# Kernel optimization log

Measured on AMD Instinct MI355X. Metric: run time of the kernel, lower is better.

## Reference

```python
import jax, jax.numpy as jnp
import numpy as np

N_NODES = 50000
N_EDGES = 800000
D = 128           # node feature / hidden / out_feature
E_FEAT = 16       # raw edge_attr dim
N_LAYERS = 3
BN_EPS = 1e-5
INV_SQRT2 = 0.7071067811865476


def setup_inputs() -> dict:
    key = jax.random.key(0)
    ks = jax.random.split(key, 12)
    x = jax.random.normal(ks[0], (N_NODES, D), dtype=jnp.float32)
    edge_index = jax.random.randint(ks[1], (2, N_EDGES), 0, N_NODES, dtype=jnp.int64)
    edge_attr = jax.random.normal(ks[2], (N_EDGES, E_FEAT), dtype=jnp.float32)
    edge_weight = jax.random.uniform(ks[3], (N_EDGES,), dtype=jnp.float32)
    # shared edge encoder (same module instance passed to every conv)
    We = jax.random.normal(ks[4], (E_FEAT, D), dtype=jnp.float32) * (1.0 / np.sqrt(E_FEAT))
    be = jnp.zeros((D,), dtype=jnp.float32)
    # per-layer MLP: Linear(D->D), GELU, Linear(D->D)
    W1 = jax.random.normal(ks[5], (N_LAYERS, D, D), dtype=jnp.float32) * (1.0 / np.sqrt(D))
    b1 = jnp.zeros((N_LAYERS, D), dtype=jnp.float32)
    W2 = jax.random.normal(ks[6], (N_LAYERS, D, D), dtype=jnp.float32) * (1.0 / np.sqrt(D))
    b2 = jnp.zeros((N_LAYERS, D), dtype=jnp.float32)
    eps = jnp.zeros((N_LAYERS,), dtype=jnp.float32)  # GINE eps params, init 0
    gamma = jnp.ones((N_LAYERS, D), dtype=jnp.float32)
    beta = jnp.zeros((N_LAYERS, D), dtype=jnp.float32)
    return {"x": x, "edge_index": edge_index, "edge_attr": edge_attr,
            "edge_weight": edge_weight, "We": We, "be": be, "W1": W1, "b1": b1,
            "W2": W2, "b2": b2, "eps": eps, "gamma": gamma, "beta": beta}


def reference(x, edge_index, edge_attr, edge_weight, We, be, W1, b1, W2, b2, eps, gamma, beta):
    src = edge_index[0]
    dst = edge_index[1]
    ew = edge_weight[:, None]                      # [E,1]
    edge_emb = edge_attr @ We + be                 # shared bond encoder, [E,D]
    n = x.shape[0]
    for i in range(N_LAYERS):
        # message: gelu(x_j + edge_emb) * edge_weight, scatter-add to dst
        m = jax.nn.gelu(x[src] + edge_emb, approximate=False) * ew   # [E,D]
        agg = jax.ops.segment_sum(m, dst, num_segments=n)            # [N,D]
        h = (1.0 + eps[i]) * x + agg
        h = jax.nn.gelu(h @ W1[i] + b1[i], approximate=False) @ W2[i] + b2[i]
        # BatchNorm1d, training mode (biased batch var)
        mu = jnp.mean(h, axis=0)
        var = jnp.var(h, axis=0)
        h = (h - mu) * jax.lax.rsqrt(var + BN_EPS) * gamma[i] + beta[i]
        h = jax.nn.gelu(h, approximate=False)
        # dropout p=0.0 -> identity; residual (shapes always match here)
        x = (x + h) * INV_SQRT2
    return x
```

## Files before the change

kernel.cpp:

```cpp
#include <hip/hip_runtime.h>
#include <math.h>

#define N_NODES 50000
#define N_EDGES 800000
#define D 128
#define E_FEAT 16
#define NLAYERS 3
#define BN_EPS 1e-5f
#define INV_SQRT2 0.70710678118654752f

typedef __attribute__((ext_vector_type(8))) short short8;
typedef __attribute__((ext_vector_type(4))) float f32x4;

__device__ __forceinline__ float gelu_fast(float v) {
    const float u = v * INV_SQRT2;
    const float a = __builtin_fabsf(u);
    const float t = __builtin_amdgcn_rcpf(__builtin_fmaf(0.3275911f, a, 1.0f));
    float p = __builtin_fmaf(1.061405429f, t, -1.453152027f);
    p = __builtin_fmaf(p, t, 1.421413741f);
    p = __builtin_fmaf(p, t, -0.284496736f);
    p = __builtin_fmaf(p, t, 0.254829592f);
    p = p * t;
    const float e = __builtin_amdgcn_exp2f(-1.4426950408889634f * a * a);
    const float erf_a = __builtin_fmaf(-p, e, 1.0f);
    const float erf_u = __builtin_copysignf(erf_a, u);
    return 0.5f * v * (1.0f + erf_u);
}

__device__ __forceinline__ unsigned short f2bf(float f) {
    unsigned u = __float_as_uint(f);
    unsigned r = (u + 0x7FFFu + ((u >> 16) & 1u)) >> 16;
    return (unsigned short)r;
}

__global__ __launch_bounds__(256) void count_kernel(const int* __restrict__ dst,
                                                    int* __restrict__ counts) {
    int e = blockIdx.x * 256 + threadIdx.x;
    if (e < N_EDGES) atomicAdd(&counts[dst[e]], 1);
}

#define NSCAN_BLOCKS 196
__global__ __launch_bounds__(256) void scan1_kernel(const int* __restrict__ counts,
                                                    int* __restrict__ offsets,
                                                    int* __restrict__ bsum) {
    __shared__ int wsum[4];
    __shared__ int wexcl[4];
    const int t = threadIdx.x, lane = t & 63, wid = t >> 6;
    const int idx = blockIdx.x * 256 + t;
    int v = (idx < N_NODES) ? counts[idx] : 0;
    int incl = v;
    #pragma unroll
    for (int off = 1; off < 64; off <<= 1) {
        int u = __shfl_up(incl, off, 64);
        if (lane >= off) incl += u;
    }
    if (lane == 63) wsum[wid] = incl;
    __syncthreads();
    if (t == 0) {
        int r = 0;
        #pragma unroll
        for (int g = 0; g < 4; ++g) { wexcl[g] = r; r += wsum[g]; }
        bsum[blockIdx.x] = r;
    }
    __syncthreads();
    if (idx < N_NODES) offsets[idx] = wexcl[wid] + (incl - v);
}

__global__ __launch_bounds__(256) void scan2_kernel(const int* __restrict__ bsum,
                                                    int* __restrict__ bbase,
                                                    int* __restrict__ offsets) {
    __shared__ int wsum[4];
    __shared__ int wexcl[4];
    const int t = threadIdx.x, lane = t & 63, wid = t >> 6;
    int v = (t < NSCAN_BLOCKS) ? bsum[t] : 0;
    int incl = v;
    #pragma unroll
    for (int off = 1; off < 64; off <<= 1) {
        int u = __shfl_up(incl, off, 64);
        if (lane >= off) incl += u;
    }
    if (lane == 63) wsum[wid] = incl;
    __syncthreads();
    if (t == 0) {
        int r = 0;
        #pragma unroll
        for (int g = 0; g < 4; ++g) { wexcl[g] = r; r += wsum[g]; }
        offsets[N_NODES] = r;
    }
    __syncthreads();
    if (t < NSCAN_BLOCKS) bbase[t] = wexcl[wid] + (incl - v);
}

__global__ __launch_bounds__(256) void scan3_kernel(int* __restrict__ offsets,
                                                    const int* __restrict__ bbase,
                                                    int* __restrict__ cursor) {
    const int idx = blockIdx.x * 256 + threadIdx.x;
    if (idx < N_NODES) {
        const int o = offsets[idx] + bbase[blockIdx.x];
        offsets[idx] = o;
        cursor[idx] = o;
    }
}

__global__ __launch_bounds__(256) void scatter_kernel(const int* __restrict__ dst,
                                                      int* __restrict__ cursor,
                                                      int* __restrict__ sorted_eid) {
    int e = blockIdx.x * 256 + threadIdx.x;
    if (e < N_EDGES) {
        int p = atomicAdd(&cursor[dst[e]], 1);
        sorted_eid[p] = e;
    }
}

__global__ __launch_bounds__(256) void permute_kernel(
    const int* __restrict__ sorted_eid,
    const int* __restrict__ src,
    const float* __restrict__ ew,
    const float* __restrict__ ea,
    int* __restrict__ sorted_src,
    float* __restrict__ sorted_ew,
    float* __restrict__ sorted_ea)
{
    int p = blockIdx.x * 256 + threadIdx.x;
    if (p < N_EDGES) {
        const int e = sorted_eid[p];
        sorted_src[p] = src[e];
        sorted_ew[p]  = ew[e];
        const float4* s4 = (const float4*)(ea + (size_t)e * E_FEAT);
        float4* d4 = (float4*)(sorted_ea + (size_t)p * E_FEAT);
        d4[0] = s4[0]; d4[1] = s4[1]; d4[2] = s4[2]; d4[3] = s4[3];
    }
}

__global__ __launch_bounds__(256) void pack_kernel(const float* __restrict__ W1,
                                                   const float* __restrict__ W2,
                                                   unsigned short* __restrict__ Wp) {
    const int idx = blockIdx.x * 256 + threadIdx.x;
    if (idx >= 6 * 2048) return;
    const int m    = idx >> 11;
    const int rem  = idx & 2047;
    const int ct   = rem >> 8;
    const int rem2 = rem & 255;
    const int kt   = rem2 >> 6;
    const int lane = rem2 & 63;
    const float* Wsrc = (m < 3) ? (W1 + (size_t)m * D * D)
                                : (W2 + (size_t)(m - 3) * D * D);
    const int k0  = kt * 32 + (lane >> 4) * 8;
    const int col = ct * 16 + (lane & 15);
    unsigned short o[8];
    #pragma unroll
    for (int j = 0; j < 8; ++j) o[j] = f2bf(Wsrc[(size_t)(k0 + j) * D + col]);
    unsigned short* d = Wp + (size_t)idx * 8;
    #pragma unroll
    for (int j = 0; j < 8; ++j) d[j] = o[j];
}

__global__ __launch_bounds__(256, 4) void aggregate_kernel(
    const float* __restrict__ x,
    const int* __restrict__ sorted_src,
    const float* __restrict__ sorted_ew,
    const float* __restrict__ sorted_ea,
    const int* __restrict__ offsets,
    const float* __restrict__ We,
    const float* __restrict__ be,
    const float* __restrict__ eps_p,
    float* __restrict__ pre)
{
    const int t = threadIdx.x;
    const int lane = t & 63;
    const int node = blockIdx.x * 4 + (t >> 6);
    const int c0 = lane * 2;

    float2 wreg[E_FEAT];
    #pragma unroll
    for (int k = 0; k < E_FEAT; ++k)
        wreg[k] = *(const float2*)&We[k * D + c0];
    const float2 bev = *(const float2*)&be[c0];
    const float e1 = 1.0f + *eps_p;

    const int start = __builtin_amdgcn_readfirstlane(offsets[node]);
    const int end   = __builtin_amdgcn_readfirstlane(offsets[node + 1]);

    float a0 = 0.0f, a1 = 0.0f;
    int p = start;
    for (; p + 2 <= end; p += 2) {
        const int s0 = __builtin_amdgcn_readfirstlane(sorted_src[p]);
        const int s1 = __builtin_amdgcn_readfirstlane(sorted_src[p + 1]);
        const float2 x0 = *(const float2*)&x[(size_t)s0 * D + c0];
        const float2 x1 = *(const float2*)&x[(size_t)s1 * D + c0];
        const float w0 = sorted_ew[p];
        const float w1 = sorted_ew[p + 1];
        const float* __restrict__ ea0 = sorted_ea + (size_t)p * E_FEAT;
        const float* __restrict__ ea1 = ea0 + E_FEAT;

        float m00 = bev.x, m01 = bev.y, m10 = bev.x, m11 = bev.y;
        #pragma unroll
        for (int k = 0; k < E_FEAT; ++k) {
            const float e0k = ea0[k];
            m00 = __builtin_fmaf(e0k, wreg[k].x, m00);
            m01 = __builtin_fmaf(e0k, wreg[k].y, m01);
        }
        #pragma unroll
        for (int k = 0; k < E_FEAT; ++k) {
            const float e1k = ea1[k];
            m10 = __builtin_fmaf(e1k, wreg[k].x, m10);
            m11 = __builtin_fmaf(e1k, wreg[k].y, m11);
        }
        a0 = __builtin_fmaf(gelu_fast(x0.x + m00), w0, a0);
        a1 = __builtin_fmaf(gelu_fast(x0.y + m01), w0, a1);
        a0 = __builtin_fmaf(gelu_fast(x1.x + m10), w1, a0);
        a1 = __builtin_fmaf(gelu_fast(x1.y + m11), w1, a1);
    }
    if (p < end) {
        const int s0 = __builtin_amdgcn_readfirstlane(sorted_src[p]);
        const float2 x0 = *(const float2*)&x[(size_t)s0 * D + c0];
        const float w0 = sorted_ew[p];
        const float* __restrict__ ea0 = sorted_ea + (size_t)p * E_FEAT;
        float m00 = bev.x, m01 = bev.y;
        #pragma unroll
        for (int k = 0; k < E_FEAT; ++k) {
            const float e0k = ea0[k];
            m00 = __builtin_fmaf(e0k, wreg[k].x, m00);
            m01 = __builtin_fmaf(e0k, wreg[k].y, m01);
        }
        a0 = __builtin_fmaf(gelu_fast(x0.x + m00), w0, a0);
        a1 = __builtin_fmaf(gelu_fast(x0.y + m01), w0, a1);
    }

    const float2 xnode = *(const float2*)&x[(size_t)node * D + c0];
    float2 o;
    o.x = e1 * xnode.x + a0;
    o.y = e1 * xnode.y + a1;
    *(float2*)&pre[(size_t)node * D + c0] = o;
}

#define GM 64
#define LDB 136

__global__ __launch_bounds__(256, 4) void mlp_fused_kernel(
    const float* __restrict__ pre,
    const unsigned short* __restrict__ Wp1,
    const float* __restrict__ b1,
    const unsigned short* __restrict__ Wp2,
    const float* __restrict__ b2,
    float* __restrict__ H,
    float* __restrict__ colsum,
    float* __restrict__ colsumsq)
{
    __shared__ __align__(16) unsigned short sAb[GM * LDB];
    __shared__ float sred[2][4][D];
    const int t = threadIdx.x;
    const int row0 = blockIdx.x * GM;

    for (int i = t; i < GM * (D / 4); i += 256) {
        const int r  = i / (D / 4);
        const int cc = (i % (D / 4)) * 4;
        const int gr = row0 + r;
        float4 v;
        if (gr < N_NODES) v = *(const float4*)&pre[(size_t)gr * D + cc];
        else { v.x = v.y = v.z = v.w = 0.0f; }
        ushort4 h;
        h.x = f2bf(v.x); h.y = f2bf(v.y); h.z = f2bf(v.z); h.w = f2bf(v.w);
        *(ushort4*)&sAb[r * LDB + cc] = h;
    }
    __syncthreads();

    const int wave = t >> 6, lane = t & 63;
    const int m0   = wave * 16;
    const int mrow = lane & 15;
    const int q    = lane >> 4;
    const int colb = lane & 15;

    short8 a[4];
    #pragma unroll
    for (int kt = 0; kt < 4; ++kt)
        a[kt] = *(const short8*)&sAb[(m0 + mrow) * LDB + kt * 32 + q * 8];

    f32x4 acc[8];
    #pragma unroll
    for (int ct = 0; ct < 8; ++ct) acc[ct] = (f32x4){0.f, 0.f, 0.f, 0.f};
    #pragma unroll
    for (int ct = 0; ct < 8; ++ct) {
        #pragma unroll
        for (int kt = 0; kt < 4; ++kt) {
            const short8 b = *(const short8*)&Wp1[((size_t)(ct * 4 + kt) * 64 + lane) * 8];
            acc[ct] = __builtin_amdgcn_mfma_f32_16x16x32_bf16(a[kt], b, acc[ct], 0, 0, 0);
        }
    }

    #pragma unroll
    for (int ct = 0; ct < 8; ++ct) {
        const float bb = b1[ct * 16 + colb];
        #pragma unroll
        for (int r = 0; r < 4; ++r) {
            const float o = gelu_fast(acc[ct][r] + bb);
            sAb[(m0 + q * 4 + r) * LDB + ct * 16 + colb] = f2bf(o);
        }
    }

    #pragma unroll
    for (int kt = 0; kt < 4; ++kt)
        a[kt] = *(const short8*)&sAb[(m0 + mrow) * LDB + kt * 32 + q * 8];
    #pragma unroll
    for (int ct = 0; ct < 8; ++ct) acc[ct] = (f32x4){0.f, 0.f, 0.f, 0.f};
    #pragma unroll
    for (int ct = 0; ct < 8; ++ct) {
        #pragma unroll
        for (int kt = 0; kt < 4; ++kt) {
            const short8 b = *(const short8*)&Wp2[((size_t)(ct * 4 + kt) * 64 + lane) * 8];
            acc[ct] = __builtin_amdgcn_mfma_f32_16x16x32_bf16(a[kt], b, acc[ct], 0, 0, 0);
        }
    }

    #pragma unroll
    for (int ct = 0; ct < 8; ++ct) {
        const float bb = b2[ct * 16 + colb];
        float ssum = 0.f, qsum = 0.f;
        #pragma unroll
        for (int r = 0; r < 4; ++r) {
            const int grow = row0 + m0 + q * 4 + r;
            const float o = acc[ct][r] + bb;
            if (grow < N_NODES) {
                H[(size_t)grow * D + ct * 16 + colb] = o;
                ssum += o;
                qsum += o * o;
            }
        }
        ssum += __shfl_xor(ssum, 16, 64);
        ssum += __shfl_xor(ssum, 32, 64);
        qsum += __shfl_xor(qsum, 16, 64);
        qsum += __shfl_xor(qsum, 32, 64);
        if (q == 0) {
            sred[0][wave][ct * 16 + colb] = ssum;
            sred[1][wave][ct * 16 + colb] = qsum;
        }
    }
    __syncthreads();
    if (t < D) {
        const float ss = sred[0][0][t] + sred[0][1][t] + sred[0][2][t] + sred[0][3][t];
        const float qq = sred[1][0][t] + sred[1][1][t] + sred[1][2][t] + sred[1][3][t];
        atomicAdd(&colsum[t], ss);
        atomicAdd(&colsumsq[t], qq);
    }
}

__global__ __launch_bounds__(256) void bn_apply_kernel(
    const float* __restrict__ H,
    const float* __restrict__ colsum,
    const float* __restrict__ colsumsq,
    const float* __restrict__ gamma,
    const float* __restrict__ beta,
    const float* __restrict__ x_in,
    float* __restrict__ x_out)
{
    const int idx = blockIdx.x * 256 + threadIdx.x;
    const int c0 = (idx & 31) * 4;
    const float invN = 1.0f / (float)N_NODES;

    const float4 s  = *(const float4*)&colsum[c0];
    const float4 q  = *(const float4*)&colsumsq[c0];
    const float4 g  = *(const float4*)&gamma[c0];
    const float4 bt = *(const float4*)&beta[c0];
    const float4 h  = *(const float4*)&H[(size_t)idx * 4];
    const float4 xv = *(const float4*)&x_in[(size_t)idx * 4];

    float4 o;
    {
        float mu = s.x * invN, var = q.x * invN - mu * mu;
        float hn = (h.x - mu) * rsqrtf(var + BN_EPS) * g.x + bt.x;
        o.x = (xv.x + gelu_fast(hn)) * INV_SQRT2;
    }
    {
        float mu = s.y * invN, var = q.y * invN - mu * mu;
        float hn = (h.y - mu) * rsqrtf(var + BN_EPS) * g.y + bt.y;
        o.y = (xv.y + gelu_fast(hn)) * INV_SQRT2;
    }
    {
        float mu = s.z * invN, var = q.z * invN - mu * mu;
        float hn = (h.z - mu) * rsqrtf(var + BN_EPS) * g.z + bt.z;
        o.z = (xv.z + gelu_fast(hn)) * INV_SQRT2;
    }
    {
        float mu = s.w * invN, var = q.w * invN - mu * mu;
        float hn = (h.w - mu) * rsqrtf(var + BN_EPS) * g.w + bt.w;
        o.w = (xv.w + gelu_fast(hn)) * INV_SQRT2;
    }
    *(float4*)&x_out[(size_t)idx * 4] = o;
}

extern "C" void kernel_launch(void* const* d_in, const int* in_sizes, int n_in,
                              void* d_out, int out_size, void* d_ws, size_t ws_size,
                              hipStream_t stream) {
    const float* x_in  = (const float*)d_in[0];
    const int*   ei    = (const int*)d_in[1];
    const float* ea    = (const float*)d_in[2];
    const float* ew    = (const float*)d_in[3];
    const float* We    = (const float*)d_in[4];
    const float* be    = (const float*)d_in[5];
    const float* W1    = (const float*)d_in[6];
    const float* b1    = (const float*)d_in[7];
    const float* W2    = (const float*)d_in[8];
    const float* b2    = (const float*)d_in[9];
    const float* eps   = (const float*)d_in[10];
    const float* gamma = (const float*)d_in[11];
    const float* beta  = (const float*)d_in[12];

    const int* src = ei;
    const int* dst = ei + N_EDGES;

    float* xcur = (float*)d_out;

    int*   counts       = (int*)d_ws;
    float* colsum_all   = (float*)(counts + N_NODES);
    float* colsumsq_all = colsum_all + NLAYERS * D;
    int*   cursor       = (int*)(colsumsq_all + NLAYERS * D);
    int*   offsets      = cursor + N_NODES;
    int*   bsum         = offsets + N_NODES + 4;
    int*   bbase        = bsum + 256;
    int*   sorted_eid   = bbase + 256;
    int*   sorted_src   = sorted_eid + N_EDGES;
    float* sorted_ew    = (float*)(sorted_src + N_EDGES);
    float* sorted_ea    = sorted_ew + N_EDGES;
    unsigned short* Wpack = (unsigned short*)(sorted_ea + (size_t)N_EDGES * E_FEAT);
    float* preH         = (float*)(Wpack + 6 * 2048 * 8);

    hipMemsetAsync(counts, 0, sizeof(int) * (N_NODES + 2 * NLAYERS * D), stream);
    count_kernel<<<(N_EDGES + 255) / 256, 256, 0, stream>>>(dst, counts);
    scan1_kernel<<<NSCAN_BLOCKS, 256, 0, stream>>>(counts, offsets, bsum);
    scan2_kernel<<<1, 256, 0, stream>>>(bsum, bbase, offsets);
    scan3_kernel<<<NSCAN_BLOCKS, 256, 0, stream>>>(offsets, bbase, cursor);
    scatter_kernel<<<(N_EDGES + 255) / 256, 256, 0, stream>>>(dst, cursor, sorted_eid);
    permute_kernel<<<(N_EDGES + 255) / 256, 256, 0, stream>>>(
        sorted_eid, src, ew, ea, sorted_src, sorted_ew, sorted_ea);
    pack_kernel<<<48, 256, 0, stream>>>(W1, W2, Wpack);

    const int mlp_blocks = (N_NODES + GM - 1) / GM;
    const int bn_blocks  = (N_NODES * D / 4) / 256;
    const int agg_blocks = N_NODES / 4;

    for (int i = 0; i < NLAYERS; ++i) {
        const float* xl = (i == 0) ? x_in : xcur;
        aggregate_kernel<<<agg_blocks, 256, 0, stream>>>(
            xl, sorted_src, sorted_ew, sorted_ea, offsets, We, be, eps + i, preH);
        mlp_fused_kernel<<<mlp_blocks, 256, 0, stream>>>(
            preH, Wpack + (size_t)i * 16384, b1 + (size_t)i * D,
            Wpack + (size_t)(3 + i) * 16384, b2 + (size_t)i * D,
            preH, colsum_all + i * D, colsumsq_all + i * D);
        bn_apply_kernel<<<bn_blocks, 256, 0, stream>>>(
            preH, colsum_all + i * D, colsumsq_all + i * D,
            gamma + (size_t)i * D, beta + (size_t)i * D, xl, xcur);
    }
}
```

Before: 690.0 us.

## Precompute bf16 edge embeddings once, use tanh GELU, store intermediates in bf16

Edge embeddings (edge_attr @ We + be) are now computed once, in a permute kernel, and stored sorted as packed bf16, so the three aggregate passes no longer redo the 16-wide dot product per edge. The aggregate kernel uses a tanh-based GELU approximation instead of the erf polynomial, and gets higher occupancy bounds. The pre-MLP and post-MLP activations are stored as bf16 instead of fp32, halving intermediate traffic. In exchange, each aggregate pass reads a 256-byte embedding per edge, the tanh GELU changes numerics relative to exact erf, and bf16 storage adds rounding error.

```diff
diff --git a/kernel.cpp b/kernel.cpp
--- a/kernel.cpp
+++ b/kernel.cpp
@@ -27,11 +27,22 @@
     return 0.5f * v * (1.0f + erf_u);
 }
 
+__device__ __forceinline__ float gelu_tanh(float x) {
+    const float x2 = x * x;
+    const float z = x * __builtin_fmaf(0.0356774081f, x2, 0.7978845608f);
+    const float E = __builtin_amdgcn_exp2f(z * 2.885390082f);
+    const float r = __builtin_amdgcn_rcpf(E + 1.0f);
+    const float th = __builtin_fmaf(-2.0f, r, 1.0f);
+    return 0.5f * x * (1.0f + th);
+}
+
 __device__ __forceinline__ unsigned short f2bf(float f) {
     unsigned u = __float_as_uint(f);
     unsigned r = (u + 0x7FFFu + ((u >> 16) & 1u)) >> 16;
     return (unsigned short)r;
 }
+__device__ __forceinline__ float bf2f_lo(unsigned u) { return __uint_as_float(u << 16); }
+__device__ __forceinline__ float bf2f_hi(unsigned u) { return __uint_as_float(u & 0xFFFF0000u); }
 
 __global__ __launch_bounds__(256) void count_kernel(const int* __restrict__ dst,
                                                     int* __restrict__ counts) {
@@ -112,23 +123,45 @@
     }
 }
 
-__global__ __launch_bounds__(256) void permute_kernel(
+#define PE_BLOCKS 2048
+#define PE_WAVES (PE_BLOCKS * 4)
+__global__ __launch_bounds__(256, 4) void permute_emb_kernel(
     const int* __restrict__ sorted_eid,
     const int* __restrict__ src,
     const float* __restrict__ ew,
     const float* __restrict__ ea,
+    const float* __restrict__ We,
+    const float* __restrict__ be,
     int* __restrict__ sorted_src,
     float* __restrict__ sorted_ew,
-    float* __restrict__ sorted_ea)
+    unsigned int* __restrict__ sorted_emb)
 {
-    int p = blockIdx.x * 256 + threadIdx.x;
-    if (p < N_EDGES) {
-        const int e = sorted_eid[p];
-        sorted_src[p] = src[e];
-        sorted_ew[p]  = ew[e];
-        const float4* s4 = (const float4*)(ea + (size_t)e * E_FEAT);
-        float4* d4 = (float4*)(sorted_ea + (size_t)p * E_FEAT);
-        d4[0] = s4[0]; d4[1] = s4[1]; d4[2] = s4[2]; d4[3] = s4[3];
+    const int t = threadIdx.x;
+    const int lane = t & 63;
+    const int gw = blockIdx.x * 4 + (t >> 6);
+    const int c0 = lane * 2;
+
+    float2 wreg[E_FEAT];
+    #pragma unroll
+    for (int k = 0; k < E_FEAT; ++k)
+        wreg[k] = *(const float2*)&We[k * D + c0];
+    const float2 bev = *(const float2*)&be[c0];
+
+    for (int p = gw; p < N_EDGES; p += PE_WAVES) {
+        const int eid = __builtin_amdgcn_readfirstlane(sorted_eid[p]);
+        const int s   = __builtin_amdgcn_readfirstlane(src[eid]);
+        const float w = ew[eid];
+        const float* __restrict__ ear = ea + (size_t)eid * E_FEAT;
+        float m0 = bev.x, m1 = bev.y;
+        #pragma unroll
+        for (int k = 0; k < E_FEAT; ++k) {
+            const float eak = ear[k];
+            m0 = __builtin_fmaf(eak, wreg[k].x, m0);
+            m1 = __builtin_fmaf(eak, wreg[k].y, m1);
+        }
+        const unsigned int packed = (unsigned int)f2bf(m0) | ((unsigned int)f2bf(m1) << 16);
+        sorted_emb[(size_t)p * 64 + lane] = packed;
+        if (lane == 0) { sorted_src[p] = s; sorted_ew[p] = w; }
     }
 }
 
@@ -155,27 +188,19 @@
     for (int j = 0; j < 8; ++j) d[j] = o[j];
 }
 
-__global__ __launch_bounds__(256, 4) void aggregate_kernel(
+__global__ __launch_bounds__(256, 8) void aggregate_kernel(
     const float* __restrict__ x,
     const int* __restrict__ sorted_src,
     const float* __restrict__ sorted_ew,
-    const float* __restrict__ sorted_ea,
+    const unsigned int* __restrict__ sorted_emb,
     const int* __restrict__ offsets,
-    const float* __restrict__ We,
-    const float* __restrict__ be,
     const float* __restrict__ eps_p,
-    float* __restrict__ pre)
+    unsigned int* __restrict__ preb)
 {
     const int t = threadIdx.x;
     const int lane = t & 63;
     const int node = blockIdx.x * 4 + (t >> 6);
     const int c0 = lane * 2;
-
-    float2 wreg[E_FEAT];
-    #pragma unroll
-    for (int k = 0; k < E_FEAT; ++k)
-        wreg[k] = *(const float2*)&We[k * D + c0];
-    const float2 bev = *(const float2*)&be[c0];
     const float e1 = 1.0f + *eps_p;
 
     const int start = __builtin_amdgcn_readfirstlane(offsets[node]);
@@ -188,62 +213,40 @@
         const int s1 = __builtin_amdgcn_readfirstlane(sorted_src[p + 1]);
         const float2 x0 = *(const float2*)&x[(size_t)s0 * D + c0];
         const float2 x1 = *(const float2*)&x[(size_t)s1 * D + c0];
+        const unsigned int e0 = sorted_emb[(size_t)p * 64 + lane];
+        const unsigned int e1u = sorted_emb[(size_t)(p + 1) * 64 + lane];
         const float w0 = sorted_ew[p];
         const float w1 = sorted_ew[p + 1];
-        const float* __restrict__ ea0 = sorted_ea + (size_t)p * E_FEAT;
-        const float* __restrict__ ea1 = ea0 + E_FEAT;
-
-        float m00 = bev.x, m01 = bev.y, m10 = bev.x, m11 = bev.y;
-        #pragma unroll
-        for (int k = 0; k < E_FEAT; ++k) {
-            const float e0k = ea0[k];
-            m00 = __builtin_fmaf(e0k, wreg[k].x, m00);
-            m01 = __builtin_fmaf(e0k, wreg[k].y, m01);
-        }
-        #pragma unroll
-        for (int k = 0; k < E_FEAT; ++k) {
-            const float e1k = ea1[k];
-            m10 = __builtin_fmaf(e1k, wreg[k].x, m10);
-            m11 = __builtin_fmaf(e1k, wreg[k].y, m11);
-        }
-        a0 = __builtin_fmaf(gelu_fast(x0.x + m00), w0, a0);
-        a1 = __builtin_fmaf(gelu_fast(x0.y + m01), w0, a1);
-        a0 = __builtin_fmaf(gelu_fast(x1.x + m10), w1, a0);
-        a1 = __builtin_fmaf(gelu_fast(x1.y + m11), w1, a1);
+        a0 = __builtin_fmaf(gelu_tanh(x0.x + bf2f_lo(e0)),  w0, a0);
+        a1 = __builtin_fmaf(gelu_tanh(x0.y + bf2f_hi(e0)),  w0, a1);
+        a0 = __builtin_fmaf(gelu_tanh(x1.x + bf2f_lo(e1u)), w1, a0);
+        a1 = __builtin_fmaf(gelu_tanh(x1.y + bf2f_hi(e1u)), w1, a1);
     }
     if (p < end) {
         const int s0 = __builtin_amdgcn_readfirstlane(sorted_src[p]);
         const float2 x0 = *(const float2*)&x[(size_t)s0 * D + c0];
+        const unsigned int e0 = sorted_emb[(size_t)p * 64 + lane];
         const float w0 = sorted_ew[p];
-        const float* __restrict__ ea0 = sorted_ea + (size_t)p * E_FEAT;
-        float m00 = bev.x, m01 = bev.y;
-        #pragma unroll
-        for (int k = 0; k < E_FEAT; ++k) {
-            const float e0k = ea0[k];
-            m00 = __builtin_fmaf(e0k, wreg[k].x, m00);
-            m01 = __builtin_fmaf(e0k, wreg[k].y, m01);
-        }
-        a0 = __builtin_fmaf(gelu_fast(x0.x + m00), w0, a0);
-        a1 = __builtin_fmaf(gelu_fast(x0.y + m01), w0, a1);
+        a0 = __builtin_fmaf(gelu_tanh(x0.x + bf2f_lo(e0)), w0, a0);
+        a1 = __builtin_fmaf(gelu_tanh(x0.y + bf2f_hi(e0)), w0, a1);
     }
 
     const float2 xnode = *(const float2*)&x[(size_t)node * D + c0];
-    float2 o;
-    o.x = e1 * xnode.x + a0;
-    o.y = e1 * xnode.y + a1;
-    *(float2*)&pre[(size_t)node * D + c0] = o;
+    const float o0 = __builtin_fmaf(e1, xnode.x, a0);
+    const float o1 = __builtin_fmaf(e1, xnode.y, a1);
+    preb[(size_t)node * 64 + lane] = (unsigned int)f2bf(o0) | ((unsigned int)f2bf(o1) << 16);
 }
 
 #define GM 64
 #define LDB 136
 
 __global__ __launch_bounds__(256, 4) void mlp_fused_kernel(
-    const float* __restrict__ pre,
+    const unsigned short* __restrict__ preb,
     const unsigned short* __restrict__ Wp1,
     const float* __restrict__ b1,
     const unsigned short* __restrict__ Wp2,
     const float* __restrict__ b2,
-    float* __restrict__ H,
+    unsigned short* __restrict__ Hb,
     float* __restrict__ colsum,
     float* __restrict__ colsumsq)
 {
@@ -252,16 +255,14 @@
     const int t = threadIdx.x;
     const int row0 = blockIdx.x * GM;
 
-    for (int i = t; i < GM * (D / 4); i += 256) {
-        const int r  = i / (D / 4);
-        const int cc = (i % (D / 4)) * 4;
+    for (int i = t; i < GM * (D / 8); i += 256) {
+        const int r  = i / (D / 8);
+        const int cc = (i % (D / 8)) * 8;
         const int gr = row0 + r;
-        float4 v;
-        if (gr < N_NODES) v = *(const float4*)&pre[(size_t)gr * D + cc];
-        else { v.x = v.y = v.z = v.w = 0.0f; }
-        ushort4 h;
-        h.x = f2bf(v.x); h.y = f2bf(v.y); h.z = f2bf(v.z); h.w = f2bf(v.w);
-        *(ushort4*)&sAb[r * LDB + cc] = h;
+        uint4 v;
+        if (gr < N_NODES) v = *(const uint4*)&preb[(size_t)gr * D + cc];
+        else { v.x = v.y = v.z = v.w = 0u; }
+        *(uint4*)&sAb[r * LDB + cc] = v;
     }
     __syncthreads();
 
@@ -321,7 +322,7 @@
             const int grow = row0 + m0 + q * 4 + r;
             const float o = acc[ct][r] + bb;
             if (grow < N_NODES) {
-                H[(size_t)grow * D + ct * 16 + colb] = o;
+                Hb[(size_t)grow * D + ct * 16 + colb] = f2bf(o);
                 ssum += o;
                 qsum += o * o;
             }
@@ -345,7 +346,7 @@
 }
 
 __global__ __launch_bounds__(256) void bn_apply_kernel(
-    const float* __restrict__ H,
+    const unsigned short* __restrict__ Hb,
     const float* __restrict__ colsum,
     const float* __restrict__ colsumsq,
     const float* __restrict__ gamma,
@@ -361,28 +362,32 @@
     const float4 q  = *(const float4*)&colsumsq[c0];
     const float4 g  = *(const float4*)&gamma[c0];
     const float4 bt = *(const float4*)&beta[c0];
-    const float4 h  = *(const float4*)&H[(size_t)idx * 4];
+    const ushort4 hb = *(const ushort4*)&Hb[(size_t)idx * 4];
     const float4 xv = *(const float4*)&x_in[(size_t)idx * 4];
 
     float4 o;
     {
+        float h = __uint_as_float((unsigned)hb.x << 16);
         float mu = s.x * invN, var = q.x * invN - mu * mu;
-        float hn = (h.x - mu) * rsqrtf(var + BN_EPS) * g.x + bt.x;
+        float hn = (h - mu) * rsqrtf(var + BN_EPS) * g.x + bt.x;
         o.x = (xv.x + gelu_fast(hn)) * INV_SQRT2;
     }
     {
+        float h = __uint_as_float((unsigned)hb.y << 16);
         float mu = s.y * invN, var = q.y * invN - mu * mu;
-        float hn = (h.y - mu) * rsqrtf(var + BN_EPS) * g.y + bt.y;
+        float hn = (h - mu) * rsqrtf(var + BN_EPS) * g.y + bt.y;
         o.y = (xv.y + gelu_fast(hn)) * INV_SQRT2;
     }
     {
+        float h = __uint_as_float((unsigned)hb.z << 16);
         float mu = s.z * invN, var = q.z * invN - mu * mu;
-        float hn = (h.z - mu) * rsqrtf(var + BN_EPS) * g.z + bt.z;
+        float hn = (h - mu) * rsqrtf(var + BN_EPS) * g.z + bt.z;
         o.z = (xv.z + gelu_fast(hn)) * INV_SQRT2;
     }
     {
+        float h = __uint_as_float((unsigned)hb.w << 16);
         float mu = s.w * invN, var = q.w * invN - mu * mu;
-        float hn = (h.w - mu) * rsqrtf(var + BN_EPS) * g.w + bt.w;
+        float hn = (h - mu) * rsqrtf(var + BN_EPS) * g.w + bt.w;
         o.w = (xv.w + gelu_fast(hn)) * INV_SQRT2;
     }
     *(float4*)&x_out[(size_t)idx * 4] = o;
@@ -420,9 +425,11 @@
     int*   sorted_eid   = bbase + 256;
     int*   sorted_src   = sorted_eid + N_EDGES;
     float* sorted_ew    = (float*)(sorted_src + N_EDGES);
-    float* sorted_ea    = sorted_ew + N_EDGES;
-    unsigned short* Wpack = (unsigned short*)(sorted_ea + (size_t)N_EDGES * E_FEAT);
-    float* preH         = (float*)(Wpack + 6 * 2048 * 8);
+    unsigned short* Wpack = (unsigned short*)(sorted_ew + N_EDGES);
+    unsigned int* sorted_emb = (unsigned int*)(Wpack + 6 * 2048 * 8);
+    unsigned int* preb_u  = sorted_emb + (size_t)N_EDGES * 64;
+    unsigned short* preb  = (unsigned short*)preb_u;
+    unsigned short* Hb    = preb;
 
     hipMemsetAsync(counts, 0, sizeof(int) * (N_NODES + 2 * NLAYERS * D), stream);
     count_kernel<<<(N_EDGES + 255) / 256, 256, 0, stream>>>(dst, counts);
@@ -430,8 +437,8 @@
     scan2_kernel<<<1, 256, 0, stream>>>(bsum, bbase, offsets);
     scan3_kernel<<<NSCAN_BLOCKS, 256, 0, stream>>>(offsets, bbase, cursor);
     scatter_kernel<<<(N_EDGES + 255) / 256, 256, 0, stream>>>(dst, cursor, sorted_eid);
-    permute_kernel<<<(N_EDGES + 255) / 256, 256, 0, stream>>>(
-        sorted_eid, src, ew, ea, sorted_src, sorted_ew, sorted_ea);
+    permute_emb_kernel<<<PE_BLOCKS, 256, 0, stream>>>(
+        sorted_eid, src, ew, ea, We, be, sorted_src, sorted_ew, sorted_emb);
     pack_kernel<<<48, 256, 0, stream>>>(W1, W2, Wpack);
 
     const int mlp_blocks = (N_NODES + GM - 1) / GM;
@@ -441,13 +448,13 @@
     for (int i = 0; i < NLAYERS; ++i) {
         const float* xl = (i == 0) ? x_in : xcur;
         aggregate_kernel<<<agg_blocks, 256, 0, stream>>>(
-            xl, sorted_src, sorted_ew, sorted_ea, offsets, We, be, eps + i, preH);
+            xl, sorted_src, sorted_ew, sorted_emb, offsets, eps + i, preb_u);
         mlp_fused_kernel<<<mlp_blocks, 256, 0, stream>>>(
-            preH, Wpack + (size_t)i * 16384, b1 + (size_t)i * D,
+            preb, Wpack + (size_t)i * 16384, b1 + (size_t)i * D,
             Wpack + (size_t)(3 + i) * 16384, b2 + (size_t)i * D,
-            preH, colsum_all + i * D, colsumsq_all + i * D);
+            Hb, colsum_all + i * D, colsumsq_all + i * D);
         bn_apply_kernel<<<bn_blocks, 256, 0, stream>>>(
-            preH, colsum_all + i * D, colsumsq_all + i * D,
+            Hb, colsum_all + i * D, colsumsq_all + i * D,
             gamma + (size_t)i * D, beta + (size_t)i * D, xl, xcur);
     }
 }
```

New measurement: 830.4 us. 20.4% more time.
